# Performance work log

Measured on AMD Instinct MI355X. Metric: run time of the kernel, lower is better.

Reference implementation:

```python
import jax, jax.numpy as jnp
import numpy as np

B, S = 512, 512
M, DK, DV, DF = 64, 128, 256, 128
NQ = 10000

def setup_inputs() -> dict:
    key = jax.random.key(0)
    ks = jax.random.split(key, 20)
    g = lambda i, sh, sc: jax.random.normal(ks[i], sh, jnp.float32) * sc
    return {
        'q_data': jax.random.randint(ks[0], (B, S), 0, NQ + 1),
        'qa_data': jax.random.randint(ks[1], (B, S), 0, 2 * NQ + 1),
        'target': jax.random.uniform(ks[2], (B * S, 1), jnp.float32),  # all >= 0 -> mask all valid
        'q_embed_w': g(3, (NQ + 1, DK), 0.1),
        'qa_embed_w': g(4, (2 * NQ + 1, DV), 0.1),
        'key_mem': g(5, (M, DK), 0.1),
        'init_value_mem': g(6, (M, DV), 0.1),
        'erase_w': g(7, (DV, DV), 0.05), 'erase_b': jnp.zeros((DV,), jnp.float32),
        'add_w': g(8, (DV, DV), 0.05), 'add_b': jnp.zeros((DV,), jnp.float32),
        'input_w': g(9, (DF, DK), 0.05), 'input_b': jnp.zeros((DF,), jnp.float32),
        'read_w': g(10, (DF, DV + DF), 0.05), 'read_b': jnp.zeros((DF,), jnp.float32),
        'predict_w': g(11, (1, DF), 0.05), 'predict_b': jnp.zeros((1,), jnp.float32),
    }


def reference(q_data, qa_data, target, q_embed_w, qa_embed_w, key_mem, init_value_mem,
              erase_w, erase_b, add_w, add_b, input_w, input_b, read_w, read_b,
              predict_w, predict_b):
    q_e = q_embed_w[q_data]      # [B,S,DK]
    qa_e = qa_embed_w[qa_data]   # [B,S,DV]

    def step(Mv, inp):
        q, qa = inp                                       # [B,DK], [B,DV]
        w = jax.nn.softmax(q @ key_mem.T, axis=-1)        # [B,M]
        read = jnp.einsum('bm,bmd->bd', w, Mv)            # [B,DV]
        erase = jax.nn.sigmoid(qa @ erase_w.T + erase_b)  # [B,DV]
        add = jnp.tanh(qa @ add_w.T + add_b)              # [B,DV]
        Mv = Mv * (1.0 - w[:, :, None] * erase[:, None, :]) + w[:, :, None] * add[:, None, :]
        return Mv, read

    Mv0 = jnp.broadcast_to(init_value_mem, (q_data.shape[0], M, DV))
    _, reads = jax.lax.scan(step, Mv0, (q_e.transpose(1, 0, 2), qa_e.transpose(1, 0, 2)))
    reads = reads.transpose(1, 0, 2)                       # [B,S,DV]

    ie = jnp.tanh(q_e @ input_w.T + input_b)               # [B,S,DF]
    rce = jnp.tanh(jnp.concatenate([reads, ie], axis=-1) @ read_w.T + read_b)
    pred = rce @ predict_w.T + predict_b                   # [B,S,1]
    pred_logit = jax.nn.sigmoid(pred)

    pred_1d = pred.reshape(-1)
    t = target.reshape(-1)
    mask = t >= 0.0
    # stable BCE-with-logits, masked mean (mask is all-True with this setup)
    bce = jnp.maximum(pred_1d, 0.0) - pred_1d * t + jnp.log1p(jnp.exp(-jnp.abs(pred_1d)))
    denom = jnp.maximum(jnp.sum(mask.astype(jnp.float32)), 1.0)
    loss = jnp.sum(jnp.where(mask, bce, 0.0)) / denom
    filtered_pred = jax.nn.sigmoid(jnp.where(mask, pred_1d, 0.0))
    filtered_target = jnp.where(mask, t, 0.0)
    return pred_logit, loss, filtered_pred, filtered_target
```

## Files before the change

### kernel.cpp

```cpp
#include <hip/hip_runtime.h>
#include <hip/hip_bf16.h>
#include <math.h>

#define BB 512
#define SS 512
#define MM 64
#define DK 128
#define DV 256
#define DF 128
#define CHUNK 16
#define NCHUNK (SS/CHUNK)

typedef __attribute__((ext_vector_type(8))) short s8v;
typedef __attribute__((ext_vector_type(4))) float f4v;
typedef __attribute__((ext_vector_type(2))) float f2v;
typedef __attribute__((ext_vector_type(8))) unsigned short u16x8;

#define MFMA16(a,b,c) __builtin_amdgcn_mfma_f32_16x16x32_bf16((a),(b),(c),0,0,0)

#define EAP_OFF 0
#define KTP_OFF 131072
#define ITP_OFF 139264
#define RTP_OFF 155648
#define WTAB_BYTE 409664
#define IET_BYTE  2969920
#define EAT_BYTE  5530176
#define WS_NEED2  26011200ull
#define READS_BYTE 26011264ull
#define WS_NEED3  (READS_BYTE + (size_t)BB*SS*DV*2)
#define PART_STRIDE_B 32768

__device__ __forceinline__ unsigned short f2bf(float x) {
    union { float f; unsigned u; } v; v.f = x;
    unsigned r = v.u + 0x7fffu + ((v.u >> 16) & 1u);
    return (unsigned short)(r >> 16);
}
__device__ __forceinline__ float bf2f(unsigned short h) {
    union { unsigned u; float f; } v; v.u = ((unsigned)h) << 16;
    return v.f;
}
__device__ __forceinline__ float u2f(unsigned u) {
    union { unsigned x; float f; } v; v.x = u; return v.f;
}
__device__ __forceinline__ float sigmoidf_(float x) { return 1.0f / (1.0f + __expf(-x)); }
__device__ __forceinline__ float fast_tanh(float x) {
    float e = __expf(2.0f * x);
    return 1.0f - 2.0f / (e + 1.0f);
}
__device__ __forceinline__ void pk_fma_acc(f2v& acc, f2v a, f2v b) {
    asm("v_pk_fma_f32 %0, %1, %2, %0" : "+v"(acc) : "v"(a), "v"(b));
}
__device__ __forceinline__ f2v pk_nfma(f2v a, f2v b, f2v c) {
    f2v d;
    asm("v_pk_fma_f32 %0, %1, %2, %3 neg_lo:[1,0,0] neg_hi:[1,0,0]"
        : "=v"(d) : "v"(a), "v"(b), "v"(c));
    return d;
}

__global__ void prep_kernel(const float* __restrict__ ew, const float* __restrict__ aw,
                            const float* __restrict__ km, const float* __restrict__ iw,
                            const float* __restrict__ rw, float* __restrict__ wsf) {
    int tid = blockIdx.x * 256 + threadIdx.x;
    int stride = gridDim.x * 256;
    if (tid < 2) wsf[tid] = 0.0f;
    unsigned short* bp = (unsigned short*)(wsf + 16);

    for (int i = tid; i < 131072; i += stride) {
        int e = i & 7, l = (i >> 3) & 63, ks = (i >> 9) & 7, nf = i >> 12;
        int k = ks*32 + (l >> 4)*8 + e;
        int n = nf*16 + (l & 15);
        float v = (n < 256) ? ew[n*DV + k] : aw[(n-256)*DV + k];
        bp[EAP_OFF + i] = f2bf(v);
    }
    for (int i = tid; i < 8192; i += stride) {
        int e = i & 7, l = (i >> 3) & 63, ks = (i >> 9) & 3, nf = i >> 11;
        int k = ks*32 + (l >> 4)*8 + e;
        int m = nf*16 + (l & 15);
        bp[KTP_OFF + i] = f2bf(km[m*DK + k]);
    }
    for (int i = tid; i < 16384; i += stride) {
        int e = i & 7, l = (i >> 3) & 63, ks = (i >> 9) & 3, nf = i >> 11;
        int k = ks*32 + (l >> 4)*8 + e;
        int f = nf*16 + (l & 15);
        bp[ITP_OFF + i] = f2bf(iw[f*DK + k]);
    }
    for (int i = tid; i < 49152; i += stride) {
        int e = i & 7, l = (i >> 3) & 63, g = i >> 9;
        int ks = g % 12, nf = g / 12;
        int j = ks*32 + (l >> 4)*8 + e;
        int f = nf*16 + (l & 15);
        bp[RTP_OFF + i] = f2bf(rw[f*(DV+DF) + j]);
    }
}

__launch_bounds__(256, 2)
__global__ void table_kernel(const float* __restrict__ q_embed, const float* __restrict__ qa_embed,
                             const float* __restrict__ erase_b, const float* __restrict__ add_b,
                             const float* __restrict__ input_b, const float* __restrict__ read_b,
                             int rw2flag, float* __restrict__ ws) {
    __shared__ __align__(128) char tsm[65536];
    const int tid  = threadIdx.x;
    const int lane = tid & 63;
    const int wave = tid >> 6;
    const int arow = lane & 15;
    const int ag   = lane >> 4;

    const unsigned short* wsb = (const unsigned short*)(ws + 16);
    const s8v* eap = (const s8v*)(wsb + EAP_OFF);
    const s8v* ktp = (const s8v*)(wsb + KTP_OFF);
    const s8v* itp = (const s8v*)(wsb + ITP_OFF);
    const s8v* rtp = (const s8v*)(wsb + RTP_OFF);
    float*          wtab = (float*)((char*)ws + WTAB_BYTE);
    unsigned short* iet  = (unsigned short*)((char*)ws + IET_BYTE);
    unsigned short* eat  = (unsigned short*)((char*)ws + EAT_BYTE);
    unsigned*       eat2 = (unsigned*)((char*)ws + EAT_BYTE);

    if (blockIdx.x < 157) {
        const int r0 = blockIdx.x * 64;
        char*  q16   = tsm;
        float* sc    = (float*)(tsm + 16384);
        unsigned short* iest = (unsigned short*)(tsm + 33792);

        #pragma unroll
        for (int it = 0; it < 8; ++it) {
            int u = it*256 + tid;
            int row = u >> 5, c4 = u & 31;
            int sr = r0 + row; if (sr > 10000) sr = 10000;
            float4 v = *(const float4*)(q_embed + sr*DK + c4*4);
            ushort4 p; p.x = f2bf(v.x); p.y = f2bf(v.y); p.z = f2bf(v.z); p.w = f2bf(v.w);
            *(ushort4*)(q16 + ((row*256 + c4*8) ^ ((row & 7) << 4))) = p;
        }
        __syncthreads();

        {
            s8v a[4];
            #pragma unroll
            for (int ks = 0; ks < 4; ++ks)
                a[ks] = *(const s8v*)(q16 + (((wave*16+arow)*256 + ks*64 + ag*16) ^ ((arow & 7) << 4)));
            #pragma unroll
            for (int j = 0; j < 4; ++j) {
                f4v cc = {0.f,0.f,0.f,0.f};
                #pragma unroll
                for (int ks = 0; ks < 4; ++ks) cc = MFMA16(a[ks], ktp[(j*4 + ks)*64 + lane], cc);
                #pragma unroll
                for (int r = 0; r < 4; ++r)
                    sc[(wave*16 + ag*4 + r)*68 + j*16 + arow] = cc[r];
            }
            __syncthreads();

            #pragma unroll
            for (int k = 0; k < 16; ++k) {
                int rr = wave*16 + k;
                float v = sc[rr*68 + lane];
                float mx = v;
                #pragma unroll
                for (int off = 32; off; off >>= 1) mx = fmaxf(mx, __shfl_xor(mx, off));
                float e = __expf(v - mx);
                float sum = e;
                #pragma unroll
                for (int off = 32; off; off >>= 1) sum += __shfl_xor(sum, off);
                if (r0 + rr < 10001) wtab[(r0 + rr)*64 + lane] = e / sum;
            }

            #pragma unroll
            for (int j = 0; j < 8; ++j) {
                f4v cc = {0.f,0.f,0.f,0.f};
                #pragma unroll
                for (int ks = 0; ks < 4; ++ks) cc = MFMA16(a[ks], itp[(j*4 + ks)*64 + lane], cc);
                float bias = input_b[j*16 + arow];
                #pragma unroll
                for (int r = 0; r < 4; ++r)
                    iest[(wave*16 + ag*4 + r)*128 + j*16 + arow] = f2bf(fast_tanh(cc[r] + bias));
            }
        }
        __syncthreads();

        if (rw2flag) {
            s8v af2[4];
            #pragma unroll
            for (int ks2 = 0; ks2 < 4; ++ks2)
                af2[ks2] = *(const s8v*)((const char*)iest + (wave*16+arow)*256 + ks2*64 + ag*16);
            f4v acc2[8];
            #pragma unroll
            for (int j = 0; j < 8; ++j) acc2[j] = (f4v){0.f,0.f,0.f,0.f};
            #pragma unroll
            for (int ks2 = 0; ks2 < 4; ++ks2)
                #pragma unroll
                for (int j = 0; j < 8; ++j)
                    acc2[j] = MFMA16(af2[ks2], rtp[(j*12 + 8 + ks2)*64 + lane], acc2[j]);
            #pragma unroll
            for (int j = 0; j < 8; ++j) {
                float rb = read_b[j*16 + arow];
                #pragma unroll
                for (int r = 0; r < 4; ++r)
                    iest[(wave*16 + ag*4 + r)*128 + j*16 + arow] = f2bf(acc2[j][r] + rb);
            }
            __syncthreads();
        }
        #pragma unroll
        for (int it = 0; it < 4; ++it) {
            int u = it*256 + tid;
            int row = u >> 4, c8 = u & 15;
            if (r0 + row < 10001)
                *(u16x8*)(iet + (r0 + row)*128 + c8*8) = *(const u16x8*)(iest + row*128 + c8*8);
        }
    } else {
        const int r0 = (blockIdx.x - 157) * 64;
        char* qa16 = tsm;

        #pragma unroll
        for (int it = 0; it < 16; ++it) {
            int u = it*256 + tid;
            int row = u >> 6, c4 = u & 63;
            int sr = r0 + row; if (sr > 20000) sr = 20000;
            float4 v = *(const float4*)(qa_embed + sr*DV + c4*4);
            ushort4 p; p.x = f2bf(v.x); p.y = f2bf(v.y); p.z = f2bf(v.z); p.w = f2bf(v.w);
            *(ushort4*)(qa16 + ((row*512 + c4*8) ^ ((row & 7) << 4))) = p;
        }
        __syncthreads();

        s8v af[8];
        #pragma unroll
        for (int ks = 0; ks < 8; ++ks)
            af[ks] = *(const s8v*)(qa16 + (((wave*16+arow)*512 + ks*64 + ag*16) ^ ((arow & 7) << 4)));

        if (rw2flag) {
            #pragma unroll
            for (int i = 0; i < 16; ++i) {
                f4v ce = {0.f,0.f,0.f,0.f}, ca = {0.f,0.f,0.f,0.f};
                #pragma unroll
                for (int ks = 0; ks < 8; ++ks) {
                    ce = MFMA16(af[ks], eap[((i     )*8 + ks)*64 + lane], ce);
                    ca = MFMA16(af[ks], eap[((i + 16)*8 + ks)*64 + lane], ca);
                }
                int n = i*16 + arow;
                float eb = erase_b[n], ab = add_b[n];
                #pragma unroll
                for (int r = 0; r < 4; ++r) {
                    int row = r0 + wave*16 + ag*4 + r;
                    unsigned u = (unsigned)f2bf(sigmoidf_(ce[r] + eb))
                               | ((unsigned)f2bf(fast_tanh(ca[r] + ab)) << 16);
                    if (row < 20001) eat2[(size_t)row*256 + n] = u;
                }
            }
        } else {
            unsigned short* east = (unsigned short*)(tsm + 32768);
            for (int h = 0; h < 2; ++h) {
                #pragma unroll
                for (int i = 0; i < 16; ++i) {
                    int nt = h*16 + i;
                    f4v cc = {0.f,0.f,0.f,0.f};
                    #pragma unroll
                    for (int ks = 0; ks < 8; ++ks) cc = MFMA16(af[ks], eap[(nt*8 + ks)*64 + lane], cc);
                    int n = nt*16 + arow;
                    float bias = (n < 256) ? erase_b[n] : add_b[n - 256];
                    #pragma unroll
                    for (int r = 0; r < 4; ++r) {
                        float v = cc[r] + bias;
                        float res = (n < 256) ? sigmoidf_(v) : fast_tanh(v);
                        east[(wave*16 + ag*4 + r)*256 + (n - h*256)] = f2bf(res);
                    }
                }
                __syncthreads();
                #pragma unroll
                for (int it = 0; it < 8; ++it) {
                    int u = it*256 + tid;
                    int row = u >> 5, c8 = u & 31;
                    if (r0 + row < 20001)
                        *(u16x8*)(eat + (size_t)(r0 + row)*512 + h*256 + c8*8) =
                            *(const u16x8*)(east + row*256 + c8*8);
                }
                __syncthreads();
            }
        }
    }
}

__launch_bounds__(256, 4)
__global__ void scan2_kernel(const int* __restrict__ q_data, const int* __restrict__ qa_data,
                             const float* __restrict__ init_mv,
                             float* __restrict__ ws) {
    __shared__ float          wf [CHUNK][68];
    __shared__ unsigned short rdp[CHUNK][4][68];

    const int bid = blockIdx.x;
    const int xcd = bid & 7, idx = bid >> 3;
    const int b   = xcd*64 + (idx >> 2);
    const int dq  = idx & 3;
    const int tid = threadIdx.x;
    const int d   = tid & 63;
    const int mq  = tid >> 6;

    const float*    wtab  = (const float*)((const char*)ws + WTAB_BYTE);
    const unsigned* eat2  = (const unsigned*)((const char*)ws + EAT_BYTE);
    unsigned short* reads = (unsigned short*)((char*)ws + READS_BYTE);

    f2v mv2[8];
    #pragma unroll
    for (int j = 0; j < 8; ++j) {
        mv2[j][0] = init_mv[(mq*16 + 2*j    )*DV + dq*64 + d];
        mv2[j][1] = init_mv[(mq*16 + 2*j + 1)*DV + dq*64 + d];
    }

    const int base = b * SS;
    const int ead  = dq*64 + d;
    const int srow = tid >> 4;
    const int wu   = tid & 15;

    int iq0, iq1;
    float4 pw;
    iq0 = q_data[base + srow];
    pw  = *(const float4*)(wtab + (size_t)iq0*64 + wu*4);
    iq1 = q_data[base + CHUNK + srow];

    for (int c = 0; c < NCHUNK; ++c) {
        *(float4*)&wf[srow][wu*4] = pw;
        __syncthreads();
        iq0 = iq1;
        if (c + 1 < NCHUNK) pw = *(const float4*)(wtab + (size_t)iq0*64 + wu*4);
        { int c2 = (c + 2 < NCHUNK) ? c + 2 : NCHUNK - 1; iq1 = q_data[base + c2*CHUNK + srow]; }

        unsigned ea[CHUNK];
        #pragma unroll
        for (int s = 0; s < CHUNK; ++s) {
            int ias = qa_data[base + c*CHUNK + s];
            ea[s] = eat2[(size_t)ias*256 + ead];
        }

        #pragma unroll
        for (int s = 0; s < CHUNK; ++s) {
            unsigned eac = ea[s];
            float e = u2f(eac << 16);
            float a = u2f(eac & 0xffff0000u);
            f2v e2; e2[0] = e; e2[1] = e;
            f2v a2; a2[0] = a; a2[1] = a;
            const f2v* wr = (const f2v*)&wf[s][mq*16];
            f2v r0 = {0.f, 0.f}, r1 = {0.f, 0.f};
            #pragma unroll
            for (int j = 0; j < 8; j += 2) {
                f2v w0 = wr[j], w1 = wr[j+1];
                pk_fma_acc(r0, w0, mv2[j]);
                f2v t0 = pk_nfma(mv2[j], e2, a2);
                pk_fma_acc(mv2[j], w0, t0);
                pk_fma_acc(r1, w1, mv2[j+1]);
                f2v t1 = pk_nfma(mv2[j+1], e2, a2);
                pk_fma_acc(mv2[j+1], w1, t1);
            }
            f2v rs = r0 + r1;
            rdp[s][mq][d] = f2bf(rs[0] + rs[1]);
        }
        __syncthreads();

        {
            int s = tid >> 4, d0 = (tid & 15) * 4;
            float a0 = 0.f, a1 = 0.f, a2 = 0.f, a3 = 0.f;
            #pragma unroll
            for (int m2 = 0; m2 < 4; ++m2) {
                ushort4 v = *(const ushort4*)&rdp[s][m2][d0];
                a0 += bf2f(v.x); a1 += bf2f(v.y); a2 += bf2f(v.z); a3 += bf2f(v.w);
            }
            ushort4 o; o.x = f2bf(a0); o.y = f2bf(a1); o.z = f2bf(a2); o.w = f2bf(a3);
            *(ushort4*)(reads + (size_t)(base + c*CHUNK + s)*DV + dq*64 + d0) = o;
        }
    }
}

__launch_bounds__(256, 2)
__global__ void rce_kernel(const int* __restrict__ q_data, const float* __restrict__ target,
                           const float* __restrict__ predict_w, const float* __restrict__ predict_b,
                           float* __restrict__ ws, float* __restrict__ out) {
    __shared__ __align__(128) char cat16[33792];
    __shared__ __align__(16) unsigned short rw2s[64][128];
    __shared__ float lred[4][2];
    float* rce_f = (float*)cat16;

    const int blk  = blockIdx.x;
    const int b    = blk >> 3;
    const int s0   = (blk & 7) * 64;
    const int tid  = threadIdx.x;
    const int lane = tid & 63;
    const int wave = tid >> 6;
    const int arow = lane & 15;
    const int ag   = lane >> 4;

    const unsigned short* wsb   = (const unsigned short*)(ws + 16);
    const s8v*            rtp   = (const s8v*)(wsb + RTP_OFF);
    const unsigned short* rw2t  = (const unsigned short*)((const char*)ws + IET_BYTE);
    const unsigned short* reads = (const unsigned short*)((const char*)ws + READS_BYTE);

    #pragma unroll
    for (int it = 0; it < 8; ++it) {
        int u = it*256 + tid, row = u >> 5, cu = u & 31;
        u16x8 v = *(const u16x8*)(reads + (size_t)(b*SS + s0 + row)*DV + cu*8);
        *(u16x8*)(cat16 + ((row*512 + cu*16) ^ ((row & 7) << 4))) = v;
    }
    #pragma unroll
    for (int it = 0; it < 4; ++it) {
        int u = it*256 + tid, row = u >> 4, cu = u & 15;
        int iq = q_data[b*SS + s0 + row];
        *(u16x8*)(&rw2s[row][cu*8]) = *(const u16x8*)(rw2t + (size_t)iq*128 + cu*8);
    }
    __syncthreads();

    f4v acc[8];
    #pragma unroll
    for (int n = 0; n < 8; ++n) acc[n] = (f4v){0.f,0.f,0.f,0.f};
    #pragma unroll
    for (int ks = 0; ks < 8; ++ks) {
        int row = wave*16 + arow;
        s8v a = *(const s8v*)(cat16 + ((row*512 + ks*64 + ag*16) ^ ((row & 7) << 4)));
        #pragma unroll
        for (int n = 0; n < 8; ++n)
            acc[n] = MFMA16(a, rtp[(n*12 + ks)*64 + lane], acc[n]);
    }
    __syncthreads();

    #pragma unroll
    for (int n = 0; n < 8; ++n) {
        #pragma unroll
        for (int r = 0; r < 4; ++r) {
            int rr = wave*16 + ag*4 + r, col = n*16 + arow;
            rce_f[rr*132 + col] = fast_tanh(acc[n][r] + bf2f(rw2s[rr][col]));
        }
    }
    __syncthreads();

    const float pw_lo = predict_w[lane];
    const float pw_hi = predict_w[lane + 64];
    float local_loss = 0.f, local_cnt = 0.f;
    #pragma unroll
    for (int k = 0; k < 16; ++k) {
        int r = wave*16 + k;
        float p = fmaf(pw_lo, rce_f[r*132 + lane], pw_hi * rce_f[r*132 + 64 + lane]);
        #pragma unroll
        for (int off = 32; off; off >>= 1) p += __shfl_xor(p, off);
        if (lane == 0) {
            p += predict_b[0];
            int gi = b*SS + s0 + r;
            float t = target[gi];
            bool mask = t >= 0.0f;
            out[gi] = sigmoidf_(p);
            out[BB*SS + 1 + gi] = sigmoidf_(mask ? p : 0.0f);
            out[2*BB*SS + 1 + gi] = mask ? t : 0.0f;
            if (mask) {
                local_loss += fmaxf(p, 0.0f) - p*t + log1pf(__expf(-fabsf(p)));
                local_cnt  += 1.0f;
            }
        }
    }
    if (lane == 0) { lred[wave][0] = local_loss; lred[wave][1] = local_cnt; }
    __syncthreads();
    if (tid == 0) {
        float L = lred[0][0] + lred[1][0] + lred[2][0] + lred[3][0];
        float C = lred[0][1] + lred[1][1] + lred[2][1] + lred[3][1];
        float* part = (float*)((char*)ws + READS_BYTE + (size_t)blk * PART_STRIDE_B);
        part[0] = L; part[1] = C;
    }
}

__global__ void finish_kernel(float* __restrict__ ws, float* __restrict__ out, int mode) {
    if (mode == 0) {
        if (threadIdx.x == 0) out[BB*SS] = ws[0] / fmaxf(ws[1], 1.0f);
        return;
    }
    __shared__ float sl[4][2];
    const int tid = threadIdx.x, lane = tid & 63, wave = tid >> 6;
    const char* base = (const char*)ws + READS_BYTE;
    float L = 0.f, C = 0.f;
    for (int i = tid; i < 4096; i += 256) {
        const float* p = (const float*)(base + (size_t)i * PART_STRIDE_B);
        L += p[0]; C += p[1];
    }
    #pragma unroll
    for (int off = 32; off; off >>= 1) {
        L += __shfl_xor(L, off);
        C += __shfl_xor(C, off);
    }
    if (lane == 0) { sl[wave][0] = L; sl[wave][1] = C; }
    __syncthreads();
    if (tid == 0) {
        float LL = sl[0][0] + sl[1][0] + sl[2][0] + sl[3][0];
        float CC = sl[0][1] + sl[1][1] + sl[2][1] + sl[3][1];
        out[BB*SS] = LL / fmaxf(CC, 1.0f);
    }
}

__launch_bounds__(512, 2)
__global__ void scan_kernel(const int* __restrict__ q_data, const int* __restrict__ qa_data,
                            const float* __restrict__ target,
                            const float* __restrict__ init_mv,
                            const float* __restrict__ read_b,
                            const float* __restrict__ predict_w, const float* __restrict__ predict_b,
                            float* __restrict__ ws, float* __restrict__ out) {
    __shared__ __align__(128) char smem[50176];
    char*           cat16 = smem;
    float*          wf    = (float*)(smem + 12288);
    unsigned short* eaL   = (unsigned short*)(smem + 16640);
    unsigned short* rdp   = (unsigned short*)(smem + 33280);
    float*          rce_f = (float*)(smem + 41728);

    const int b    = blockIdx.x;
    const int tid  = threadIdx.x;
    const int lane = tid & 63;
    const int wave = tid >> 6;
    const int arow = lane & 15;
    const int ag   = lane >> 4;
    const int d    = tid & 255;
    const int half = tid >> 8;

    const unsigned short* wsb = (const unsigned short*)(ws + 16);
    const s8v* rtp = (const s8v*)(wsb + RTP_OFF);
    const float*          wtab = (const float*)((const char*)ws + WTAB_BYTE);
    const unsigned short* iet  = (const unsigned short*)((const char*)ws + IET_BYTE);
    const unsigned short* eat  = (const unsigned short*)((const char*)ws + EAT_BYTE);

    float mv[32];
    #pragma unroll
    for (int i = 0; i < 32; ++i) mv[i] = init_mv[(half*32 + i)*DV + d];

    const float rb    = read_b[wave*16 + arow];
    const float pw_lo = predict_w[lane];
    const float pw_hi = predict_w[lane + 64];

    const int base  = b * SS;
    const int erow  = tid >> 5;
    const int eunit = tid & 31;
    const int role  = tid >> 8;
    const int grow  = (tid >> 4) & 15;
    const int gunit = tid & 15;

    int iqa0, iq0, iqa1, iq1;
    u16x8 pe0, pe1, pie;
    float4 pwf;

    auto loadidx = [&](int cc, int& xa, int& xq) {
        xa = qa_data[base + cc*CHUNK + erow];
        xq = q_data [base + cc*CHUNK + grow];
    };
    auto loadrows = [&]() {
        const unsigned short* er_ptr = eat + (size_t)iqa0*512 + eunit*16;
        pe0 = *(const u16x8*)(er_ptr);
        pe1 = *(const u16x8*)(er_ptr + 8);
        if (role == 0) pwf = *(const float4*)(wtab + iq0*64 + gunit*4);
        else           pie = *(const u16x8*)(iet + (size_t)iq0*128 + gunit*8);
    };
    auto storerows = [&]() {
        *(u16x8*)(eaL + erow*520 + eunit*16)     = pe0;
        *(u16x8*)(eaL + erow*520 + eunit*16 + 8) = pe1;
        if (role == 0) *(float4*)((char*)wf + grow*272 + gunit*16) = pwf;
        else *(u16x8*)(cat16 + ((grow*768 + 512 + gunit*16) ^ ((grow & 7) << 4))) = pie;
    };

    loadidx(0, iqa0, iq0);
    loadrows();
    loadidx(1, iqa1, iq1);

    float local_loss = 0.0f, local_cnt = 0.0f;

    for (int c = 0; c < NCHUNK; ++c) {
        storerows();
        __syncthreads();
        iqa0 = iqa1; iq0 = iq1;
        if (c + 1 < NCHUNK) loadrows();
        { int c2 = (c + 2 < NCHUNK) ? c + 2 : NCHUNK - 1; loadidx(c2, iqa1, iq1); }

        for (int s = 0; s < CHUNK; ++s) {
            float e = bf2f(eaL[s*520 + d]);
            float a = bf2f(eaL[s*520 + 256 + d]);
            const float4* wr4 = (const float4*)(wf + s*68 + half*32);
            float r0 = 0.f, r1 = 0.f, r2 = 0.f, r3 = 0.f;
            #pragma unroll
            for (int j = 0; j < 8; ++j) {
                float4 w = wr4[j];
                r0 = fmaf(w.x, mv[j*4+0], r0); mv[j*4+0] = fmaf(w.x, fmaf(-mv[j*4+0], e, a), mv[j*4+0]);
                r1 = fmaf(w.y, mv[j*4+1], r1); mv[j*4+1] = fmaf(w.y, fmaf(-mv[j*4+1], e, a), mv[j*4+1]);
                r2 = fmaf(w.z, mv[j*4+2], r2); mv[j*4+2] = fmaf(w.z, fmaf(-mv[j*4+2], e, a), mv[j*4+2]);
                r3 = fmaf(w.w, mv[j*4+3], r3); mv[j*4+3] = fmaf(w.w, fmaf(-mv[j*4+3], e, a), mv[j*4+3]);
            }
            float rd = (r0 + r1) + (r2 + r3);
            if (half == 0) {
                *(unsigned short*)(cat16 + ((s*768 + d*2) ^ ((s & 7) << 4))) = f2bf(rd);
            } else {
                rdp[s*264 + d] = f2bf(rd);
            }
        }
        __syncthreads();

        if (half == 0) {
            #pragma unroll
            for (int s = 0; s < CHUNK; ++s) {
                unsigned short* p = (unsigned short*)(cat16 + ((s*768 + d*2) ^ ((s & 7) << 4)));
                *p = f2bf(bf2f(*p) + bf2f(rdp[s*264 + d]));
            }
        }
        __syncthreads();

        {
            f4v cc = {0.f,0.f,0.f,0.f};
            #pragma unroll
            for (int ks = 0; ks < 12; ++ks) {
                s8v a = *(const s8v*)(cat16 + ((arow*768 + ks*64 + ag*16) ^ ((arow & 7) << 4)));
                cc = MFMA16(a, rtp[(wave*12 + ks)*64 + lane], cc);
            }
            #pragma unroll
            for (int r = 0; r < 4; ++r)
                rce_f[(ag*4 + r)*132 + wave*16 + arow] = fast_tanh(cc[r] + rb);
        }
        __syncthreads();

        #pragma unroll
        for (int k = 0; k < 2; ++k) {
            int r = wave*2 + k;
            float p = fmaf(pw_lo, rce_f[r*132 + lane], pw_hi * rce_f[r*132 + 64 + lane]);
            #pragma unroll
            for (int off = 32; off; off >>= 1) p += __shfl_xor(p, off);
            if (lane == 0) {
                p += predict_b[0];
                int gi = b*SS + c*CHUNK + r;
                float t = target[gi];
                bool mask = t >= 0.0f;
                out[gi] = sigmoidf_(p);
                float pm = mask ? p : 0.0f;
                out[BB*SS + 1 + gi] = sigmoidf_(pm);
                out[2*BB*SS + 1 + gi] = mask ? t : 0.0f;
                if (mask) {
                    local_loss += fmaxf(p, 0.0f) - p*t + log1pf(__expf(-fabsf(p)));
                    local_cnt  += 1.0f;
                }
            }
        }
    }

    #pragma unroll
    for (int off = 32; off; off >>= 1) {
        local_loss += __shfl_xor(local_loss, off);
        local_cnt  += __shfl_xor(local_cnt, off);
    }
    if (lane == 0) {
        atomicAdd(&ws[0], local_loss);
        atomicAdd(&ws[1], local_cnt);
    }
}

extern "C" void kernel_launch(void* const* d_in, const int* in_sizes, int n_in,
                              void* d_out, int out_size, void* d_ws, size_t ws_size,
                              hipStream_t stream) {
    const int*   q_data    = (const int*)d_in[0];
    const int*   qa_data   = (const int*)d_in[1];
    const float* target    = (const float*)d_in[2];
    const float* q_embed   = (const float*)d_in[3];
    const float* qa_embed  = (const float*)d_in[4];
    const float* key_mem   = (const float*)d_in[5];
    const float* init_mv   = (const float*)d_in[6];
    const float* erase_w   = (const float*)d_in[7];
    const float* erase_b   = (const float*)d_in[8];
    const float* add_w     = (const float*)d_in[9];
    const float* add_b     = (const float*)d_in[10];
    const float* input_w   = (const float*)d_in[11];
    const float* input_b   = (const float*)d_in[12];
    const float* read_w    = (const float*)d_in[13];
    const float* read_b    = (const float*)d_in[14];
    const float* predict_w = (const float*)d_in[15];
    const float* predict_b = (const float*)d_in[16];

    float* ws  = (float*)d_ws;
    float* out = (float*)d_out;

    hipLaunchKernelGGL(prep_kernel, dim3(256), dim3(256), 0, stream,
                       erase_w, add_w, key_mem, input_w, read_w, ws);
    if (ws_size >= WS_NEED3) {
        hipLaunchKernelGGL(table_kernel, dim3(470), dim3(256), 0, stream,
                           q_embed, qa_embed, erase_b, add_b, input_b, read_b, 1, ws);
        hipLaunchKernelGGL(scan2_kernel, dim3(2048), dim3(256), 0, stream,
                           q_data, qa_data, init_mv, ws);
        hipLaunchKernelGGL(rce_kernel, dim3(4096), dim3(256), 0, stream,
                           q_data, target, predict_w, predict_b, ws, out);
        hipLaunchKernelGGL(finish_kernel, dim3(1), dim3(256), 0, stream, ws, out, 1);
    } else {
        hipLaunchKernelGGL(table_kernel, dim3(470), dim3(256), 0, stream,
                           q_embed, qa_embed, erase_b, add_b, input_b, read_b, 0, ws);
        hipLaunchKernelGGL(scan_kernel, dim3(BB), dim3(512), 0, stream,
                           q_data, qa_data, target, init_mv,
                           read_b, predict_w, predict_b, ws, out);
        hipLaunchKernelGGL(finish_kernel, dim3(1), dim3(256), 0, stream, ws, out, 0);
    }
}
```

Measured before the change: 565.7 us.

## Stage erase/add rows in LDS and read softmax weights via scalar loads

The scan kernel now prefetches the per-step erase/add rows cooperatively into shared memory with coalesced vector loads, instead of each thread issuing sixteen scattered scalar gathers per chunk. The attention weights are read straight from global memory through a wave-uniform offset, so the compiler can use scalar loads rather than staging them in LDS. The packed-FMA inline asm is replaced with scalar fmaf over a float array. The aim is to cut gather latency and LDS traffic in the serial recurrence. In exchange there are per-step scalar loads of q_data and weights on the dependent path, and the packed-math throughput is lost.

```diff
diff --git a/kernel.cpp b/kernel.cpp
--- a/kernel.cpp
+++ b/kernel.cpp
@@ -13,7 +13,6 @@
 
 typedef __attribute__((ext_vector_type(8))) short s8v;
 typedef __attribute__((ext_vector_type(4))) float f4v;
-typedef __attribute__((ext_vector_type(2))) float f2v;
 typedef __attribute__((ext_vector_type(8))) unsigned short u16x8;
 
 #define MFMA16(a,b,c) __builtin_amdgcn_mfma_f32_16x16x32_bf16((a),(b),(c),0,0,0)
@@ -46,15 +45,6 @@
 __device__ __forceinline__ float fast_tanh(float x) {
     float e = __expf(2.0f * x);
     return 1.0f - 2.0f / (e + 1.0f);
-}
-__device__ __forceinline__ void pk_fma_acc(f2v& acc, f2v a, f2v b) {
-    asm("v_pk_fma_f32 %0, %1, %2, %0" : "+v"(acc) : "v"(a), "v"(b));
-}
-__device__ __forceinline__ f2v pk_nfma(f2v a, f2v b, f2v c) {
-    f2v d;
-    asm("v_pk_fma_f32 %0, %1, %2, %3 neg_lo:[1,0,0] neg_hi:[1,0,0]"
-        : "=v"(d) : "v"(a), "v"(b), "v"(c));
-    return d;
 }
 
 __global__ void prep_kernel(const float* __restrict__ ew, const float* __restrict__ aw,
@@ -280,7 +270,7 @@
 __global__ void scan2_kernel(const int* __restrict__ q_data, const int* __restrict__ qa_data,
                              const float* __restrict__ init_mv,
                              float* __restrict__ ws) {
-    __shared__ float          wf [CHUNK][68];
+    __shared__ unsigned       eaL[CHUNK][68];
     __shared__ unsigned short rdp[CHUNK][4][68];
 
     const int bid = blockIdx.x;
@@ -290,64 +280,51 @@
     const int tid = threadIdx.x;
     const int d   = tid & 63;
     const int mq  = tid >> 6;
+    const int mqs = __builtin_amdgcn_readfirstlane(mq);
 
     const float*    wtab  = (const float*)((const char*)ws + WTAB_BYTE);
     const unsigned* eat2  = (const unsigned*)((const char*)ws + EAT_BYTE);
     unsigned short* reads = (unsigned short*)((char*)ws + READS_BYTE);
 
-    f2v mv2[8];
-    #pragma unroll
-    for (int j = 0; j < 8; ++j) {
-        mv2[j][0] = init_mv[(mq*16 + 2*j    )*DV + dq*64 + d];
-        mv2[j][1] = init_mv[(mq*16 + 2*j + 1)*DV + dq*64 + d];
-    }
+    float mv[16];
+    #pragma unroll
+    for (int j = 0; j < 16; ++j) mv[j] = init_mv[(mqs*16 + j)*DV + dq*64 + d];
 
     const int base = b * SS;
-    const int ead  = dq*64 + d;
     const int srow = tid >> 4;
-    const int wu   = tid & 15;
-
-    int iq0, iq1;
-    float4 pw;
-    iq0 = q_data[base + srow];
-    pw  = *(const float4*)(wtab + (size_t)iq0*64 + wu*4);
-    iq1 = q_data[base + CHUNK + srow];
+    const int sun  = tid & 15;
+
+    int ia0, ia1;
+    uint4 pe;
+    ia0 = qa_data[base + srow];
+    pe  = *(const uint4*)(eat2 + (size_t)ia0*256 + dq*64 + sun*4);
+    ia1 = qa_data[base + CHUNK + srow];
 
     for (int c = 0; c < NCHUNK; ++c) {
-        *(float4*)&wf[srow][wu*4] = pw;
-        __syncthreads();
-        iq0 = iq1;
-        if (c + 1 < NCHUNK) pw = *(const float4*)(wtab + (size_t)iq0*64 + wu*4);
-        { int c2 = (c + 2 < NCHUNK) ? c + 2 : NCHUNK - 1; iq1 = q_data[base + c2*CHUNK + srow]; }
-
-        unsigned ea[CHUNK];
+        *(uint4*)&eaL[srow][sun*4] = pe;
+        __syncthreads();
+        ia0 = ia1;
+        if (c + 1 < NCHUNK) pe = *(const uint4*)(eat2 + (size_t)ia0*256 + dq*64 + sun*4);
+        { int c2 = (c + 2 < NCHUNK) ? c + 2 : NCHUNK - 1; ia1 = qa_data[base + c2*CHUNK + srow]; }
+
         #pragma unroll
         for (int s = 0; s < CHUNK; ++s) {
-            int ias = qa_data[base + c*CHUNK + s];
-            ea[s] = eat2[(size_t)ias*256 + ead];
-        }
-
-        #pragma unroll
-        for (int s = 0; s < CHUNK; ++s) {
-            unsigned eac = ea[s];
+            unsigned eac = eaL[s][d];
             float e = u2f(eac << 16);
             float a = u2f(eac & 0xffff0000u);
-            f2v e2; e2[0] = e; e2[1] = e;
-            f2v a2; a2[0] = a; a2[1] = a;
-            const f2v* wr = (const f2v*)&wf[s][mq*16];
-            f2v r0 = {0.f, 0.f}, r1 = {0.f, 0.f};
-            #pragma unroll
-            for (int j = 0; j < 8; j += 2) {
-                f2v w0 = wr[j], w1 = wr[j+1];
-                pk_fma_acc(r0, w0, mv2[j]);
-                f2v t0 = pk_nfma(mv2[j], e2, a2);
-                pk_fma_acc(mv2[j], w0, t0);
-                pk_fma_acc(r1, w1, mv2[j+1]);
-                f2v t1 = pk_nfma(mv2[j+1], e2, a2);
-                pk_fma_acc(mv2[j+1], w1, t1);
-            }
-            f2v rs = r0 + r1;
-            rdp[s][mq][d] = f2bf(rs[0] + rs[1]);
+            int iqs = q_data[base + c*CHUNK + s];
+            int woff = __builtin_amdgcn_readfirstlane(iqs*64 + mqs*16);
+            const float* __restrict__ wrow = wtab + woff;
+            float r0 = 0.f, r1 = 0.f, r2 = 0.f, r3 = 0.f;
+            #pragma unroll
+            for (int j = 0; j < 16; j += 4) {
+                float w0 = wrow[j], w1 = wrow[j+1], w2 = wrow[j+2], w3 = wrow[j+3];
+                r0 = fmaf(w0, mv[j  ], r0); mv[j  ] = fmaf(w0, fmaf(-mv[j  ], e, a), mv[j  ]);
+                r1 = fmaf(w1, mv[j+1], r1); mv[j+1] = fmaf(w1, fmaf(-mv[j+1], e, a), mv[j+1]);
+                r2 = fmaf(w2, mv[j+2], r2); mv[j+2] = fmaf(w2, fmaf(-mv[j+2], e, a), mv[j+2]);
+                r3 = fmaf(w3, mv[j+3], r3); mv[j+3] = fmaf(w3, fmaf(-mv[j+3], e, a), mv[j+3]);
+            }
+            rdp[s][mq][d] = f2bf((r0 + r1) + (r2 + r3));
         }
         __syncthreads();
 
```

Result: slower. 924.8 us (+63.5%).
